# Performance work log

Measured on AMD Instinct MI355X. Metric: run time of the kernel, lower is better.

## Reference

```python
import jax, jax.numpy as jnp
import numpy as np

DIM = 512
H_RES, W_RES = 64, 64
NUM_HEADS = 16
WS = 8            # window_size
SS = 4            # shift_size
MLP_RATIO = 4
BATCH = 32
N_WIN_TOK = WS * WS


def _rel_pos_index(ws):
    coords = np.stack(np.meshgrid(np.arange(ws), np.arange(ws), indexing='ij'))  # [2, ws, ws]
    cf = coords.reshape(2, -1)
    rel = cf[:, :, None] - cf[:, None, :]          # [2, N, N]
    rel = rel.transpose(1, 2, 0).astype(np.int64)  # [N, N, 2]
    rel[..., 0] += ws - 1
    rel[..., 1] += ws - 1
    rel[..., 0] *= 2 * ws - 1
    return rel.sum(-1)                             # [N, N]


def _shift_attn_mask(H, W, ws, ss):
    # zone labeling for cyclic-shift masking (computed at trace time, static)
    img = np.zeros((H, W), dtype=np.float32)
    cnt = 0
    for hs in (slice(0, -ws), slice(-ws, -ss), slice(-ss, None)):
        for wsl in (slice(0, -ws), slice(-ws, -ss), slice(-ss, None)):
            img[hs, wsl] = cnt
            cnt += 1
    win = img.reshape(H // ws, ws, W // ws, ws).transpose(0, 2, 1, 3).reshape(-1, ws * ws)  # [nW, N]
    diff = win[:, None, :] - win[:, :, None]
    return np.where(diff != 0, -100.0, 0.0).astype(np.float32)  # [nW, N, N]


def layer_norm(x, g, b, eps=1e-5):
    mu = jnp.mean(x, axis=-1, keepdims=True)
    var = jnp.var(x, axis=-1, keepdims=True)
    return (x - mu) * jax.lax.rsqrt(var + eps) * g + b


def setup_inputs() -> dict:
    key = jax.random.key(0)
    ks = jax.random.split(key, 16)
    C, Ch = DIM, DIM * MLP_RATIO
    s = lambda k, *shape: jax.random.normal(k, shape, dtype=jnp.float32) * 0.02
    return {
        'x': jax.random.normal(ks[0], (BATCH, H_RES * W_RES, C), dtype=jnp.float32),
        'norm1_g': jnp.ones((C,), jnp.float32), 'norm1_b': jnp.zeros((C,), jnp.float32),
        'qkv_w': s(ks[1], 3 * C, C), 'qkv_b': jnp.zeros((3 * C,), jnp.float32),
        'proj_w': s(ks[2], C, C), 'proj_b': jnp.zeros((C,), jnp.float32),
        'rpb_table': s(ks[3], (2 * WS - 1) ** 2, NUM_HEADS),
        'norm2_g': jnp.ones((C,), jnp.float32), 'norm2_b': jnp.zeros((C,), jnp.float32),
        'fc1_w': s(ks[4], Ch, C), 'fc1_b': jnp.zeros((Ch,), jnp.float32),
        'fc2_w': s(ks[5], C, Ch), 'fc2_b': jnp.zeros((C,), jnp.float32),
    }


def reference(x, norm1_g, norm1_b, qkv_w, qkv_b, proj_w, proj_b, rpb_table,
              norm2_g, norm2_b, fc1_w, fc1_b, fc2_w, fc2_b):
    B, L, C = x.shape
    H, W = H_RES, W_RES
    nH = NUM_HEADS
    hd = C // nH
    N = N_WIN_TOK

    rpi = _rel_pos_index(WS)                       # static [N, N]
    attn_mask = jnp.asarray(_shift_attn_mask(H, W, WS, SS))  # [nW, N, N]

    shortcut = x
    h = layer_norm(x, norm1_g, norm1_b).reshape(B, H, W, C)
    h = jnp.roll(h, (-SS, -SS), axis=(1, 2))       # cyclic shift

    # window partition -> [B*nW, N, C]
    nWh, nWw = H // WS, W // WS
    hw = h.reshape(B, nWh, WS, nWw, WS, C).transpose(0, 1, 3, 2, 4, 5).reshape(-1, N, C)
    B_ = hw.shape[0]

    qkv = hw @ qkv_w.T + qkv_b                     # [B_, N, 3C]
    qkv = qkv.reshape(B_, N, 3, nH, hd).transpose(2, 0, 3, 1, 4)
    q, k, v = qkv[0], qkv[1], qkv[2]               # each [B_, nH, N, hd]

    scale = hd ** -0.5
    attn = jnp.einsum('bhnd,bhmd->bhnm', q * scale, k)  # [B_, nH, N, N]

    bias = rpb_table[rpi.reshape(-1)].reshape(N, N, nH).transpose(2, 0, 1)
    attn = attn + bias[None]

    nW = attn_mask.shape[0]
    attn = attn.reshape(B_ // nW, nW, nH, N, N) + attn_mask[None, :, None]
    attn = attn.reshape(B_, nH, N, N)
    attn = jax.nn.softmax(attn, axis=-1)

    out = jnp.einsum('bhnm,bhmd->bhnd', attn, v).transpose(0, 2, 1, 3).reshape(B_, N, C)
    out = out @ proj_w.T + proj_b

    # window reverse + reverse shift
    out = out.reshape(B, nWh, nWw, WS, WS, C).transpose(0, 1, 3, 2, 4, 5).reshape(B, H, W, C)
    out = jnp.roll(out, (SS, SS), axis=(1, 2)).reshape(B, L, C)

    x = shortcut + out
    m = layer_norm(x, norm2_g, norm2_b)
    m = jax.nn.gelu(m @ fc1_w.T + fc1_b, approximate=False) @ fc2_w.T + fc2_b
    return x + m
```

## Files before the change

kernel.cpp:

```cpp
#include <hip/hip_runtime.h>
#include <cstdint>

typedef __bf16 bf16;
typedef bf16 bf16x8 __attribute__((ext_vector_type(8)));
typedef bf16 bf16x4 __attribute__((ext_vector_type(4)));
typedef float f32x4 __attribute__((ext_vector_type(4)));

#define DEVI __device__ __forceinline__

DEVI void gload_lds16(const void* g, void* l) {
  typedef __attribute__((address_space(1))) void gas_t;
  typedef __attribute__((address_space(3))) void las_t;
  __builtin_amdgcn_global_load_lds((gas_t*)g, (las_t*)l, 16, 0, 0);
}

__global__ void cast_w(const float* __restrict__ in, bf16* __restrict__ out, int n) {
  int i = (blockIdx.x * 256 + threadIdx.x) * 4;
  if (i >= n) return;
  f32x4 v = *(const f32x4*)(in + i);
  bf16x4 o;
#pragma unroll
  for (int j = 0; j < 4; j++) o[j] = (bf16)v[j];
  *(bf16x4*)(out + i) = o;
}

template<bool PERM>
__global__ __launch_bounds__(256, 4) void ln_bf16(
    const float* __restrict__ in, const float* __restrict__ gam,
    const float* __restrict__ bet, bf16* __restrict__ out)
{
  const int row = blockIdx.x * 4 + (threadIdx.x >> 6);
  const int lane = threadIdx.x & 63;
  size_t src;
  if constexpr (PERM) {
    const int rem = row & 4095, w = rem >> 6, t = rem & 63;
    const int r0 = ((w >> 3) * 8 + (t >> 3) + 4) & 63;
    const int c0 = ((w & 7) * 8 + (t & 7) + 4) & 63;
    src = ((size_t)(row >> 12) * 4096 + r0 * 64 + c0) * 512;
  } else {
    src = (size_t)row * 512;
  }
  const f32x4 v0 = *(const f32x4*)(in + src + lane * 8);
  const f32x4 v1 = *(const f32x4*)(in + src + lane * 8 + 4);
  float s  = v0[0] + v0[1] + v0[2] + v0[3] + v1[0] + v1[1] + v1[2] + v1[3];
  float sq = v0[0]*v0[0] + v0[1]*v0[1] + v0[2]*v0[2] + v0[3]*v0[3]
           + v1[0]*v1[0] + v1[1]*v1[1] + v1[2]*v1[2] + v1[3]*v1[3];
#pragma unroll
  for (int m = 1; m < 64; m <<= 1) { s += __shfl_xor(s, m, 64); sq += __shfl_xor(sq, m, 64); }
  const float mean = s * 0.001953125f;
  const float rstd = rsqrtf(sq * 0.001953125f - mean * mean + 1e-5f);
  const f32x4 g0 = *(const f32x4*)(gam + lane * 8), g1 = *(const f32x4*)(gam + lane * 8 + 4);
  const f32x4 b0 = *(const f32x4*)(bet + lane * 8), b1 = *(const f32x4*)(bet + lane * 8 + 4);
  bf16x8 o;
#pragma unroll
  for (int j = 0; j < 4; j++) o[j]     = (bf16)((v0[j] - mean) * rstd * g0[j] + b0[j]);
#pragma unroll
  for (int j = 0; j < 4; j++) o[4 + j] = (bf16)((v1[j] - mean) * rstd * g1[j] + b1[j]);
  *(bf16x8*)(out + (size_t)row * 512 + lane * 8) = o;
}

constexpr int M_QKV = 0, M_PROJ = 1, M_FC1 = 2, M_FC2 = 3;

template<int MODE>
__global__ __launch_bounds__(256, 2) void gemm_bt(
    const bf16* __restrict__ A, const bf16* __restrict__ W,
    const float* __restrict__ bias, void* __restrict__ Cout,
    const float* __restrict__ extra, int N, int K, int ldc)
{
  __shared__ bf16 sA[4096];
  __shared__ bf16 sB[4096];
  const int nN = N >> 7;
  const unsigned nwg = gridDim.x;
  const unsigned id = (blockIdx.x & 7) * (nwg >> 3) + (blockIdx.x >> 3);
  const int bn = id % nN;
  const int bm = id / nN;
  const int lane = threadIdx.x & 63;
  const int wave = threadIdx.x >> 6;
  const int wr = wave >> 1, wc = wave & 1;
  const size_t m0 = (size_t)bm * 128, n0 = (size_t)bn * 128;

  f32x4 acc[4][4] = {};

  for (int k0 = 0; k0 < K; k0 += 32) {
    __syncthreads();
#pragma unroll
    for (int c = wave; c < 8; c += 4) {
      const int u = c * 64 + lane;
      const int rr = u & 127, kg = u >> 7;
      gload_lds16(A + (m0 + rr) * K + k0 + kg * 8, (char*)sA + c * 1024);
      gload_lds16(W + (n0 + rr) * K + k0 + kg * 8, (char*)sB + c * 1024);
    }
    __syncthreads();
    bf16x8 af[4], bw[4];
#pragma unroll
    for (int i = 0; i < 4; i++) {
      af[i] = *(const bf16x8*)&sA[(lane >> 4) * 1024 + (wr * 64 + i * 16 + (lane & 15)) * 8];
      bw[i] = *(const bf16x8*)&sB[(lane >> 4) * 1024 + (wc * 64 + i * 16 + (lane & 15)) * 8];
    }
#pragma unroll
    for (int i = 0; i < 4; i++)
#pragma unroll
      for (int j = 0; j < 4; j++)
        acc[i][j] = __builtin_amdgcn_mfma_f32_16x16x32_bf16(af[i], bw[j], acc[i][j], 0, 0, 0);
  }

  const int colb = (int)n0 + wc * 64 + (lane & 15);
  const int rowb = (int)m0 + wr * 64 + ((lane >> 4) << 2);
#pragma unroll
  for (int j = 0; j < 4; j++) {
    const int col = colb + j * 16;
    const float bv = bias[col];
#pragma unroll
    for (int i = 0; i < 4; i++) {
#pragma unroll
      for (int r = 0; r < 4; r++) {
        const int row = rowb + i * 16 + r;
        float v = acc[i][j][r] + bv;
        if constexpr (MODE == M_QKV) {
          ((bf16*)Cout)[(size_t)row * ldc + col] = (bf16)v;
        } else if constexpr (MODE == M_FC1) {
          v = 0.5f * v * (1.0f + erff(v * 0.70710678118f));
          ((bf16*)Cout)[(size_t)row * ldc + col] = (bf16)v;
        } else if constexpr (MODE == M_PROJ) {
          const int rem = row & 4095, w = rem >> 6, t = rem & 63;
          const int r0 = ((w >> 3) * 8 + (t >> 3) + 4) & 63;
          const int c0 = ((w & 7) * 8 + (t & 7) + 4) & 63;
          const size_t idx = ((size_t)(row >> 12) * 4096 + r0 * 64 + c0) * 512 + col;
          ((float*)Cout)[idx] = extra[idx] + v;
        } else {
          const size_t idx = (size_t)row * 512 + col;
          ((float*)Cout)[idx] = extra[idx] + v;
        }
      }
    }
  }
}

DEVI int zone3(int r) { return r < 56 ? 0 : (r < 60 ? 1 : 2); }

__global__ __launch_bounds__(256, 2) void attn_win(
    const bf16* __restrict__ qkv, const float* __restrict__ rpb, bf16* __restrict__ out)
{
  __shared__ bf16 sP[4][1024];
  __shared__ bf16 sVt[2048];
  const int tid = threadIdx.x;
  const int lane = tid & 63, wave = tid >> 6;
  const int win = blockIdx.x >> 4, h = blockIdx.x & 15;
  const size_t base = (size_t)win * 64;
  const int wi = win & 63, wh = wi >> 3, ww = wi & 7;

  {
    const int vrow = tid >> 2, cg = tid & 3;
    const bf16x8 v = *(const bf16x8*)(qkv + (base + vrow) * 1536 + 1024 + h * 32 + cg * 8);
#pragma unroll
    for (int j = 0; j < 8; j++) {
      const int d = cg * 8 + j;
      *(bf16*)((char*)sVt + ((d * 128 + vrow * 2) ^ ((d & 7) << 4))) = v[j];
    }
  }

  const bf16x8 qf = *(const bf16x8*)(qkv + (base + wave * 16 + (lane & 15)) * 1536 + h * 32 + (lane >> 4) * 8);
  bf16x8 kf[4];
#pragma unroll
  for (int ct = 0; ct < 4; ct++)
    kf[ct] = *(const bf16x8*)(qkv + (base + ct * 16 + (lane & 15)) * 1536 + 512 + h * 32 + (lane >> 4) * 8);

  const f32x4 fzero = {0.f, 0.f, 0.f, 0.f};
  f32x4 s[4];
#pragma unroll
  for (int ct = 0; ct < 4; ct++)
    s[ct] = __builtin_amdgcn_mfma_f32_16x16x32_bf16(qf, kf[ct], fzero, 0, 0, 0);

  char* Pw = (char*)sP[wave];
#pragma unroll
  for (int r = 0; r < 4; r++) {
    const int qloc = (lane >> 4) * 4 + r;
    const int t1 = wave * 16 + qloc;
    const int th1 = t1 >> 3, tw1 = t1 & 7;
    const int z1 = zone3(wh * 8 + th1) * 3 + zone3(ww * 8 + tw1);
    float z[4];
#pragma unroll
    for (int ct = 0; ct < 4; ct++) {
      const int t2 = ct * 16 + (lane & 15);
      const int th2 = t2 >> 3, tw2 = t2 & 7;
      const int z2 = zone3(wh * 8 + th2) * 3 + zone3(ww * 8 + tw2);
      const float bvv = rpb[((th1 - th2 + 7) * 15 + (tw1 - tw2 + 7)) * 16 + h];
      z[ct] = s[ct][r] * 0.17677669529663687f + bvv + (z1 != z2 ? -100.0f : 0.0f);
    }
    float mx = fmaxf(fmaxf(z[0], z[1]), fmaxf(z[2], z[3]));
#pragma unroll
    for (int msk = 1; msk < 16; msk <<= 1) mx = fmaxf(mx, __shfl_xor(mx, msk, 64));
    float p[4], sum = 0.f;
#pragma unroll
    for (int ct = 0; ct < 4; ct++) { p[ct] = __expf(z[ct] - mx); sum += p[ct]; }
#pragma unroll
    for (int msk = 1; msk < 16; msk <<= 1) sum += __shfl_xor(sum, msk, 64);
    const float inv = 1.0f / sum;
#pragma unroll
    for (int ct = 0; ct < 4; ct++) {
      const int t2 = ct * 16 + (lane & 15);
      *(bf16*)(Pw + ((qloc * 128 + t2 * 2) ^ ((qloc & 7) << 4))) = (bf16)(p[ct] * inv);
    }
  }

  __syncthreads();

  f32x4 o[2] = {};
#pragma unroll
  for (int ks = 0; ks < 2; ks++) {
    const bf16x8 pa = *(const bf16x8*)(Pw +
        (((lane & 15) * 128 + ks * 64 + (lane >> 4) * 16) ^ (((lane & 15) & 7) << 4)));
#pragma unroll
    for (int dt = 0; dt < 2; dt++) {
      const int d = dt * 16 + (lane & 15);
      const bf16x8 vb = *(const bf16x8*)((char*)sVt +
          ((d * 128 + ks * 64 + (lane >> 4) * 16) ^ ((d & 7) << 4)));
      o[dt] = __builtin_amdgcn_mfma_f32_16x16x32_bf16(pa, vb, o[dt], 0, 0, 0);
    }
  }
#pragma unroll
  for (int dt = 0; dt < 2; dt++)
#pragma unroll
    for (int r = 0; r < 4; r++) {
      const size_t row = base + wave * 16 + (lane >> 4) * 4 + r;
      out[row * 512 + h * 32 + dt * 16 + (lane & 15)] = (bf16)o[dt][r];
    }
}

extern "C" void kernel_launch(void* const* d_in, const int* in_sizes, int n_in,
                              void* d_out, int out_size, void* d_ws, size_t ws_size,
                              hipStream_t stream) {
  (void)in_sizes; (void)n_in; (void)out_size; (void)ws_size;
  const float* x      = (const float*)d_in[0];
  const float* n1g    = (const float*)d_in[1];
  const float* n1b    = (const float*)d_in[2];
  const float* qkv_w  = (const float*)d_in[3];
  const float* qkv_b  = (const float*)d_in[4];
  const float* proj_w = (const float*)d_in[5];
  const float* proj_b = (const float*)d_in[6];
  const float* rpb    = (const float*)d_in[7];
  const float* n2g    = (const float*)d_in[8];
  const float* n2b    = (const float*)d_in[9];
  const float* fc1_w  = (const float*)d_in[10];
  const float* fc1_b  = (const float*)d_in[11];
  const float* fc2_w  = (const float*)d_in[12];
  const float* fc2_b  = (const float*)d_in[13];
  float* out = (float*)d_out;

  char* ws = (char*)d_ws;
  bf16* wqkv  = (bf16*)ws;
  bf16* wproj = wqkv  + 1536 * 512;
  bf16* wfc1  = wproj + 512 * 512;
  bf16* wfc2  = wfc1  + 2048 * 512;
  size_t off = 2ull * (1536 * 512 + 512 * 512 + 2048 * 512 + 512 * 2048);
  bf16* R1 = (bf16*)(ws + off);  off += (size_t)131072 * 512 * 2;
  float* x1 = (float*)(ws + off); off += (size_t)131072 * 512 * 4;
  bf16* R2 = (bf16*)(ws + off);

  cast_w<<<768,  256, 0, stream>>>(qkv_w,  wqkv, 1536 * 512);
  cast_w<<<256,  256, 0, stream>>>(proj_w, wproj, 512 * 512);
  cast_w<<<1024, 256, 0, stream>>>(fc1_w,  wfc1, 2048 * 512);
  cast_w<<<1024, 256, 0, stream>>>(fc2_w,  wfc2, 512 * 2048);

  ln_bf16<true><<<32768, 256, 0, stream>>>(x, n1g, n1b, R1);
  gemm_bt<M_QKV><<<12288, 256, 0, stream>>>(R1, wqkv, qkv_b, R2, nullptr, 1536, 512, 1536);
  attn_win<<<32768, 256, 0, stream>>>(R2, rpb, R1);
  gemm_bt<M_PROJ><<<4096, 256, 0, stream>>>(R1, wproj, proj_b, x1, x, 512, 512, 512);
  ln_bf16<false><<<32768, 256, 0, stream>>>(x1, n2g, n2b, R1);
  gemm_bt<M_FC1><<<16384, 256, 0, stream>>>(R1, wfc1, fc1_b, R2, nullptr, 2048, 512, 2048);
  gemm_bt<M_FC2><<<4096, 256, 0, stream>>>(R2, wfc2, fc2_b, out, x1, 512, 2048, 512);
}
```

Measured before the change: 3.035 ms.

## Triple-buffer GEMM LDS loads and stage epilogue through LDS for vector stores

```diff
diff --git a/kernel.cpp b/kernel.cpp
--- a/kernel.cpp
+++ b/kernel.cpp
@@ -13,6 +13,10 @@
   typedef __attribute__((address_space(3))) void las_t;
   __builtin_amdgcn_global_load_lds((gas_t*)g, (las_t*)l, 16, 0, 0);
 }
+
+#define WAITBAR(N) asm volatile("s_waitcnt vmcnt(" #N ")\n\ts_barrier" ::: "memory")
+#define ENDBAR()   asm volatile("s_barrier" ::: "memory")
+#define LGKMBAR()  asm volatile("s_waitcnt lgkmcnt(0)\n\ts_barrier" ::: "memory")
 
 __global__ void cast_w(const float* __restrict__ in, bf16* __restrict__ out, int n) {
   int i = (blockIdx.x * 256 + threadIdx.x) * 4;
@@ -67,8 +71,7 @@
     const float* __restrict__ bias, void* __restrict__ Cout,
     const float* __restrict__ extra, int N, int K, int ldc)
 {
-  __shared__ bf16 sA[4096];
-  __shared__ bf16 sB[4096];
+  __shared__ char smem[49152] __attribute__((aligned(16)));
   const int nN = N >> 7;
   const unsigned nwg = gridDim.x;
   const unsigned id = (blockIdx.x & 7) * (nwg >> 3) + (blockIdx.x >> 3);
@@ -78,61 +81,109 @@
   const int wave = threadIdx.x >> 6;
   const int wr = wave >> 1, wc = wave & 1;
   const size_t m0 = (size_t)bm * 128, n0 = (size_t)bn * 128;
+  const int T = K >> 5;
 
   f32x4 acc[4][4] = {};
 
-  for (int k0 = 0; k0 < K; k0 += 32) {
-    __syncthreads();
-#pragma unroll
-    for (int c = wave; c < 8; c += 4) {
+  auto STAGE = [&](int t, int buf) {
+    const int kb = t << 5;
+    char* base = smem + buf * 16384;
+#pragma unroll
+    for (int cc = 0; cc < 2; cc++) {
+      const int c = wave + cc * 4;
       const int u = c * 64 + lane;
       const int rr = u & 127, kg = u >> 7;
-      gload_lds16(A + (m0 + rr) * K + k0 + kg * 8, (char*)sA + c * 1024);
-      gload_lds16(W + (n0 + rr) * K + k0 + kg * 8, (char*)sB + c * 1024);
-    }
-    __syncthreads();
+      gload_lds16(A + (m0 + rr) * K + kb + kg * 8, base + c * 1024);
+      gload_lds16(W + (n0 + rr) * K + kb + kg * 8, base + 8192 + c * 1024);
+    }
+  };
+
+  auto COMPUTE = [&](int buf) {
+    const bf16* sAb = (const bf16*)(smem + buf * 16384);
+    const bf16* sBb = sAb + 4096;
     bf16x8 af[4], bw[4];
 #pragma unroll
     for (int i = 0; i < 4; i++) {
-      af[i] = *(const bf16x8*)&sA[(lane >> 4) * 1024 + (wr * 64 + i * 16 + (lane & 15)) * 8];
-      bw[i] = *(const bf16x8*)&sB[(lane >> 4) * 1024 + (wc * 64 + i * 16 + (lane & 15)) * 8];
+      af[i] = *(const bf16x8*)&sAb[(lane >> 4) * 1024 + (wr * 64 + i * 16 + (lane & 15)) * 8];
+      bw[i] = *(const bf16x8*)&sBb[(lane >> 4) * 1024 + (wc * 64 + i * 16 + (lane & 15)) * 8];
     }
 #pragma unroll
     for (int i = 0; i < 4; i++)
 #pragma unroll
       for (int j = 0; j < 4; j++)
         acc[i][j] = __builtin_amdgcn_mfma_f32_16x16x32_bf16(af[i], bw[j], acc[i][j], 0, 0, 0);
-  }
-
-  const int colb = (int)n0 + wc * 64 + (lane & 15);
-  const int rowb = (int)m0 + wr * 64 + ((lane >> 4) << 2);
-#pragma unroll
-  for (int j = 0; j < 4; j++) {
-    const int col = colb + j * 16;
-    const float bv = bias[col];
-#pragma unroll
-    for (int i = 0; i < 4; i++) {
-#pragma unroll
-      for (int r = 0; r < 4; r++) {
-        const int row = rowb + i * 16 + r;
-        float v = acc[i][j][r] + bv;
-        if constexpr (MODE == M_QKV) {
-          ((bf16*)Cout)[(size_t)row * ldc + col] = (bf16)v;
-        } else if constexpr (MODE == M_FC1) {
-          v = 0.5f * v * (1.0f + erff(v * 0.70710678118f));
-          ((bf16*)Cout)[(size_t)row * ldc + col] = (bf16)v;
-        } else if constexpr (MODE == M_PROJ) {
-          const int rem = row & 4095, w = rem >> 6, t = rem & 63;
-          const int r0 = ((w >> 3) * 8 + (t >> 3) + 4) & 63;
-          const int c0 = ((w & 7) * 8 + (t & 7) + 4) & 63;
-          const size_t idx = ((size_t)(row >> 12) * 4096 + r0 * 64 + c0) * 512 + col;
-          ((float*)Cout)[idx] = extra[idx] + v;
-        } else {
-          const size_t idx = (size_t)row * 512 + col;
-          ((float*)Cout)[idx] = extra[idx] + v;
+  };
+
+  STAGE(0, 0);
+  STAGE(1, 1);
+  int bs = 2, bc = 0;
+  for (int t = 0; t < T - 2; ++t) {
+    STAGE(t + 2, bs);
+    WAITBAR(8);
+    COMPUTE(bc);
+    ENDBAR();
+    bs = bs + 1 < 3 ? bs + 1 : 0;
+    bc = bc + 1 < 3 ? bc + 1 : 0;
+  }
+  WAITBAR(4);  COMPUTE(bc);  ENDBAR();
+  bc = bc + 1 < 3 ? bc + 1 : 0;
+  WAITBAR(0);  COMPUTE(bc);  ENDBAR();
+
+  float* sc = (float*)smem;
+  const int lgrp = lane >> 4, lid = lane & 15;
+#pragma unroll
+  for (int h = 0; h < 2; ++h) {
+    if (wr == h) {
+#pragma unroll
+      for (int i = 0; i < 4; i++)
+#pragma unroll
+        for (int j = 0; j < 4; j++)
+#pragma unroll
+          for (int r = 0; r < 4; r++)
+            sc[(i * 16 + lgrp * 4 + r) * 132 + wc * 64 + j * 16 + lid] = acc[i][j][r];
+    }
+    LGKMBAR();
+#pragma unroll
+    for (int it = 0; it < 8; it++) {
+      const int ch = threadIdx.x + it * 256;
+      const int lr = ch >> 5, c4 = (ch & 31) * 4;
+      f32x4 v = *(const f32x4*)&sc[lr * 132 + c4];
+      const int gm = (int)m0 + h * 64 + lr;
+      const int gn = (int)n0 + c4;
+      const f32x4 bv = *(const f32x4*)(bias + gn);
+      if constexpr (MODE == M_QKV) {
+        bf16x4 o;
+#pragma unroll
+        for (int j = 0; j < 4; j++) o[j] = (bf16)(v[j] + bv[j]);
+        *(bf16x4*)((bf16*)Cout + (size_t)gm * ldc + gn) = o;
+      } else if constexpr (MODE == M_FC1) {
+        bf16x4 o;
+#pragma unroll
+        for (int j = 0; j < 4; j++) {
+          const float z = v[j] + bv[j];
+          o[j] = (bf16)(0.5f * z * (1.0f + erff(z * 0.70710678118f)));
         }
+        *(bf16x4*)((bf16*)Cout + (size_t)gm * ldc + gn) = o;
+      } else if constexpr (MODE == M_PROJ) {
+        const int rem = gm & 4095, w = rem >> 6, t = rem & 63;
+        const int r0 = ((w >> 3) * 8 + (t >> 3) + 4) & 63;
+        const int c0 = ((w & 7) * 8 + (t & 7) + 4) & 63;
+        const size_t idx = ((size_t)(gm >> 12) * 4096 + r0 * 64 + c0) * 512 + gn;
+        const f32x4 e = *(const f32x4*)(extra + idx);
+        f32x4 o;
+#pragma unroll
+        for (int j = 0; j < 4; j++) o[j] = e[j] + v[j] + bv[j];
+        *(f32x4*)((float*)Cout + idx) = o;
+      } else {
+        const size_t idx = (size_t)gm * 512 + gn;
+        const f32x4 e = *(const f32x4*)(extra + idx);
+        f32x4 o;
+#pragma unroll
+        for (int j = 0; j < 4; j++) o[j] = e[j] + v[j] + bv[j];
+        *(f32x4*)((float*)Cout + idx) = o;
       }
     }
+    if (h == 0) ENDBAR();
   }
 }
 
```

New measurement: 2.759 ms. 9.1% less time.
